# Performance work log

Measured on AMD Instinct MI355X. Metric: run time of the kernel, lower is better.

## Reference

```python
import jax, jax.numpy as jnp
import numpy as np

N_NODES = 100000
N_REL = 8
IN_DIM = 64
HID = 128
OUT = 64
N_EDGES = 640000


def setup_inputs() -> dict:
    key = jax.random.key(0)
    ks = jax.random.split(key, 24)

    def w(k, shape, fan_in):
        return jax.random.normal(k, shape, jnp.float32) / np.sqrt(fan_in).astype(np.float32)

    inp = {}
    inp["emb"] = jax.random.normal(ks[0], (N_NODES, IN_DIM), jnp.float32)
    dims = [(IN_DIM, HID), (HID, HID), (HID, HID // 2), (HID // 2, OUT)]
    for i, (di, do) in enumerate(dims, 1):
        inp[f"W{i}"] = w(ks[3 * i], (N_REL, di, do), di)      # per-relation weight
        inp[f"R{i}"] = w(ks[3 * i + 1], (di, do), di)          # root weight
        inp[f"B{i}"] = jnp.zeros((do,), jnp.float32)           # bias
    inp["g1"] = jnp.ones((HID,), jnp.float32)
    inp["b1"] = jnp.zeros((HID,), jnp.float32)
    inp["g2"] = jnp.ones((HID,), jnp.float32)
    inp["b2"] = jnp.zeros((HID,), jnp.float32)
    inp["ei"] = jax.random.randint(ks[20], (2, N_EDGES), 0, N_NODES, jnp.int32)
    inp["et"] = jax.random.randint(ks[21], (N_EDGES,), 0, N_REL, jnp.int32)
    return inp


def rgcn(x, ei, et, W, Wr, b):
    # PyG RGCNConv (aggr='mean'): out_i = x_i @ Wroot + b + sum_r mean_{j in N_r(i)} x_j @ W_r
    # Aggregate-then-transform: mean x[src] per (dst, rel) bin, then per-relation GEMM.
    n, r, d = x.shape[0], W.shape[0], x.shape[1]
    src, dst = ei[0], ei[1]
    seg = dst * r + et                                   # combined (node, relation) segment id
    agg = jax.ops.segment_sum(x[src], seg, num_segments=n * r)          # [N*R, d]
    cnt = jax.ops.segment_sum(jnp.ones((src.shape[0],), x.dtype), seg, num_segments=n * r)
    agg = (agg / jnp.maximum(cnt, 1.0)[:, None]).reshape(n, r, d)       # mean per relation
    return jnp.einsum('nri,rio->no', agg, W) + x @ Wr + b


def layer_norm(x, g, b, eps=1e-5):
    mu = jnp.mean(x, axis=-1, keepdims=True)
    var = jnp.mean((x - mu) ** 2, axis=-1, keepdims=True)
    return (x - mu) * jax.lax.rsqrt(var + eps) * g + b


def reference(emb, W1, R1, B1, W2, R2, B2, W3, R3, B3, W4, R4, B4, g1, b1, g2, b2, ei, et):
    # dropout is eval-mode identity
    x = jax.nn.relu(rgcn(emb, ei, et, W1, R1, B1))
    x = layer_norm(x, g1, b1)
    identity = x
    x = jax.nn.relu(rgcn(x, ei, et, W2, R2, B2))
    x = layer_norm(x + identity, g2, b2)
    x = jax.nn.relu(rgcn(x, ei, et, W3, R3, B3))
    return rgcn(x, ei, et, W4, R4, B4)
```

## Files before the change

kernel.cpp:

```cpp
#include <hip/hip_runtime.h>
#include <math.h>

#define NN 100000
#define NR 8
#define NE 640000
#define SEGN (NN * NR)
#define SPB 2048
#define NSB ((SEGN + SPB - 1) / SPB)

#define QSZ 25024
static const int qbase[5] = {0, 25024, 50048, 75072, 100032};
static const int qsize[4] = {25024, 25024, 25024, 24960};

typedef __attribute__((ext_vector_type(8))) __bf16 bf16x8;
typedef __attribute__((ext_vector_type(4))) float  f32x4;

__device__ __forceinline__ float bf2f(unsigned short b) {
    return __uint_as_float((unsigned)b << 16);
}
__device__ __forceinline__ unsigned short f2bf(float v) {
    __bf16 b = (__bf16)v;
    return __builtin_bit_cast(unsigned short, b);
}


__global__ __launch_bounds__(256) void count_kernel(
    const int* __restrict__ dst, const int* __restrict__ et, unsigned* __restrict__ cnt) {
    int e = blockIdx.x * 256 + threadIdx.x;
    if (e < NE) atomicAdd(&cnt[(size_t)et[e] * NN + dst[e]], 1u);
}

__global__ __launch_bounds__(256) void scan1_kernel(
    const unsigned* __restrict__ cnt, unsigned* __restrict__ bsum) {
    __shared__ unsigned red[256];
    int b = blockIdx.x, t = threadIdx.x;
    int i0 = b * SPB;
    unsigned s = 0;
#pragma unroll
    for (int k = 0; k < SPB / 256; ++k) {
        int i = i0 + k * 256 + t;
        if (i < SEGN) s += cnt[i];
    }
    red[t] = s;
    __syncthreads();
    for (int off = 128; off >= 1; off >>= 1) {
        if (t < off) red[t] += red[t + off];
        __syncthreads();
    }
    if (t == 0) bsum[b] = red[0];
}

__global__ __launch_bounds__(512) void scan2_kernel(
    unsigned* __restrict__ bsum, int* __restrict__ segoff) {
    __shared__ unsigned buf[512];
    int t = threadIdx.x;
    unsigned v = (t < NSB) ? bsum[t] : 0u;
    buf[t] = v;
    __syncthreads();
    for (int off = 1; off < 512; off <<= 1) {
        unsigned w = (t >= off) ? buf[t - off] : 0u;
        __syncthreads();
        buf[t] += w;
        __syncthreads();
    }
    if (t < NSB) bsum[t] = buf[t] - v;
    if (t == 0) segoff[SEGN] = NE;
}

__global__ __launch_bounds__(256) void scan3_kernel(
    const unsigned* __restrict__ cnt, const unsigned* __restrict__ bsum,
    int* __restrict__ segoff) {
    __shared__ unsigned lc[SPB];
    __shared__ unsigned tsum[256];
    int b = blockIdx.x, t = threadIdx.x;
    int i0 = b * SPB;
#pragma unroll
    for (int k = 0; k < SPB / 256; ++k) {
        int i = i0 + k * 256 + t;
        lc[k * 256 + t] = (i < SEGN) ? cnt[i] : 0u;
    }
    __syncthreads();
    unsigned s = 0;
#pragma unroll
    for (int k = 0; k < 8; ++k) s += lc[t * 8 + k];
    tsum[t] = s;
    __syncthreads();
    for (int off = 1; off < 256; off <<= 1) {
        unsigned w = (t >= off) ? tsum[t - off] : 0u;
        __syncthreads();
        tsum[t] += w;
        __syncthreads();
    }
    unsigned base = bsum[b] + tsum[t] - s;
#pragma unroll
    for (int k = 0; k < 8; ++k) {
        unsigned c = lc[t * 8 + k];
        lc[t * 8 + k] = base;
        base += c;
    }
    __syncthreads();
#pragma unroll
    for (int k = 0; k < SPB / 256; ++k) {
        int i = i0 + k * 256 + t;
        if (i < SEGN) segoff[i] = (int)lc[k * 256 + t];
    }
}

__global__ __launch_bounds__(256) void fill_kernel(
    const int* __restrict__ src, const int* __restrict__ dst, const int* __restrict__ et,
    const int* __restrict__ segoff, unsigned* __restrict__ cursor, int* __restrict__ esrc) {
    int e = blockIdx.x * 256 + threadIdx.x;
    if (e >= NE) return;
    int d = dst[e];
    int seg = et[e] * NN + d;
    int pos = segoff[seg] + (int)atomicAdd(&cursor[seg], 1u);
    esrc[pos] = src[e] | ((d & 3) << 17);
}

__global__ __launch_bounds__(256) void conv_emb(
    const float* __restrict__ emb, ushort* __restrict__ embb) {
    int i = blockIdx.x * 256 + threadIdx.x;
    if (i * 4 >= NN * 64) return;
    f32x4 v = *(const f32x4*)(emb + (size_t)i * 4);
    ushort4 o;
    o.x = f2bf(v[0]); o.y = f2bf(v[1]); o.z = f2bf(v[2]); o.w = f2bf(v[3]);
    *(ushort4*)(embb + (size_t)i * 4) = o;
}


template <int D, int O>
__global__ __launch_bounds__(256) void pack_kernel(
    const float* __restrict__ W, const float* __restrict__ Wr, __bf16* __restrict__ Wp) {
    constexpr int KT = D / 32, NTN = O / 16;
    int idx = blockIdx.x * 256 + threadIdx.x;
    if (idx >= (NR + 1) * KT * NTN * 64) return;
    int l = idx & 63;
    int rest = idx >> 6;
    int nt = rest % NTN; rest /= NTN;
    int kt = rest % KT;
    int r  = rest / KT;
    const float* srcw = (r < NR) ? (W + (size_t)r * D * O) : Wr;
    int n  = nt * 16 + (l & 15);
    int k0 = kt * 32 + (l >> 4) * 8;
    bf16x8 v;
#pragma unroll
    for (int j = 0; j < 8; ++j) {
        int p  = k0 + j;
        int kd = (D == 128) ? ((p >> 1) + ((p & 1) << 6)) : p;
        v[j] = (__bf16)srcw[(size_t)kd * O + n];
    }
    *(bf16x8*)(Wp + (size_t)idx * 8) = v;
}


template <int D, int O, int MODE, int XF, int OF>
__global__ __launch_bounds__(256) void fused_kernel(
    int mb,
    const ushort* __restrict__ aggG, const __bf16* __restrict__ Wp,
    const float* __restrict__ bias, const float* __restrict__ gamma,
    const float* __restrict__ beta, const unsigned* __restrict__ xres,
    const void* __restrict__ xroot, void* __restrict__ outv, int gbase, int gQP,
    const void* __restrict__ xin, const int* __restrict__ segoff,
    const int* __restrict__ esrc, ushort* __restrict__ aggS, int nbase, int sQP)
{
    constexpr int KT = D / 32, NTN = O / 16;
    int tid = threadIdx.x;
    int wv = tid >> 6, ln = tid & 63;

    if ((int)blockIdx.x < mb) {
        constexpr int PD = (D == 64) ? 8 : 3;
        int lg = ln >> 4, lm = ln & 15;
        int i0 = blockIdx.x * 64 + wv * 16;

        const ushort* abase = aggG + ((size_t)(i0 + lm)) * D + lg * 8;

        bf16x8 Aall[NR][KT];
#pragma unroll
        for (int r = 0; r < PD; ++r) {
            const ushort* ar = abase + (size_t)r * gQP * D;
#pragma unroll
            for (int kt = 0; kt < KT; ++kt)
                Aall[r][kt] = *(const bf16x8*)(ar + kt * 32);
        }

        bf16x8 Aroot[KT];
        {
            int nrow = gbase + i0 + lm;
            if (nrow >= NN) nrow = NN - 1;
#pragma unroll
            for (int kt = 0; kt < KT; ++kt) {
                if constexpr (XF == 1) {
                    Aroot[kt] = *(const bf16x8*)((const ushort*)xroot +
                                                 (size_t)nrow * 128 + kt * 32 + lg * 8);
                } else {
                    Aroot[kt] = *(const bf16x8*)((const ushort*)xroot +
                                                 (size_t)nrow * 64 + kt * 32 + lg * 8);
                }
            }
        }

        f32x4 acc[NTN];
#pragma unroll
        for (int nt = 0; nt < NTN; ++nt)
#pragma unroll
            for (int q = 0; q < 4; ++q) acc[nt][q] = 0.0f;

#pragma unroll
        for (int r = 0; r < NR; ++r) {
            if (r + PD < NR) {
                const ushort* an = abase + (size_t)(r + PD) * gQP * D;
#pragma unroll
                for (int kt = 0; kt < KT; ++kt)
                    Aall[r + PD][kt] = *(const bf16x8*)(an + kt * 32);
            }
            const __bf16* bp = Wp + (((size_t)(r * KT) * NTN) << 9) + (ln << 3);
#pragma unroll
            for (int kt = 0; kt < KT; ++kt) {
                const __bf16* bpk = bp + (((size_t)(kt * NTN)) << 9);
#pragma unroll
                for (int nt = 0; nt < NTN; ++nt) {
                    bf16x8 B = *(const bf16x8*)(bpk + ((size_t)nt << 9));
                    acc[nt] = __builtin_amdgcn_mfma_f32_16x16x32_bf16(Aall[r][kt], B, acc[nt], 0, 0, 0);
                }
            }
        }
        {
            const __bf16* bp = Wp + (((size_t)(8 * KT) * NTN) << 9) + (ln << 3);
#pragma unroll
            for (int kt = 0; kt < KT; ++kt) {
                const __bf16* bpk = bp + (((size_t)(kt * NTN)) << 9);
#pragma unroll
                for (int nt = 0; nt < NTN; ++nt) {
                    bf16x8 B = *(const bf16x8*)(bpk + ((size_t)nt << 9));
                    acc[nt] = __builtin_amdgcn_mfma_f32_16x16x32_bf16(Aroot[kt], B, acc[nt], 0, 0, 0);
                }
            }
        }

        float bb[NTN], gg[NTN], be[NTN];
#pragma unroll
        for (int nt = 0; nt < NTN; ++nt) {
            bb[nt] = bias[nt * 16 + lm];
            if constexpr (MODE <= 1) {
                gg[nt] = gamma[nt * 16 + lm];
                be[nt] = beta[nt * 16 + lm];
            } else {
                gg[nt] = 0.0f; be[nt] = 0.0f;
            }
        }
#pragma unroll
        for (int q = 0; q < 4; ++q) {
            int row = lg * 4 + q;
            int n = gbase + i0 + row;
            int nc = (n < NN) ? n : 0;
            float v[NTN];
#pragma unroll
            for (int nt = 0; nt < NTN; ++nt) {
                v[nt] = acc[nt][q] + bb[nt];
                if constexpr (MODE <= 2) v[nt] = fmaxf(v[nt], 0.0f);
                if constexpr (MODE == 1) {
                    unsigned w = xres[(size_t)nc * 64 + (nt & 3) * 16 + lm];
                    v[nt] += bf2f((unsigned short)((nt < 4) ? (w & 0xFFFFu) : (w >> 16)));
                }
            }
            if constexpr (MODE <= 1) {
                float s1 = 0.0f, s2 = 0.0f;
#pragma unroll
                for (int nt = 0; nt < NTN; ++nt) { s1 += v[nt]; s2 += v[nt] * v[nt]; }
#pragma unroll
                for (int off = 1; off < 16; off <<= 1) {
                    s1 += __shfl_xor(s1, off, 64);
                    s2 += __shfl_xor(s2, off, 64);
                }
                float mu  = s1 * (1.0f / O);
                float var = s2 * (1.0f / O) - mu * mu;
                float rs  = rsqrtf(var + 1e-5f);
#pragma unroll
                for (int nt = 0; nt < NTN; ++nt) v[nt] = (v[nt] - mu) * rs * gg[nt] + be[nt];
            }
            if (n < NN) {
                if constexpr (OF == 0) {
#pragma unroll
                    for (int nt = 0; nt < NTN; ++nt)
                        __builtin_nontemporal_store(
                            v[nt], (float*)outv + (size_t)n * O + nt * 16 + lm);
                } else if constexpr (OF == 1) {
#pragma unroll
                    for (int nt = 0; nt < 4; ++nt)
                        ((unsigned*)outv)[(size_t)n * 64 + nt * 16 + lm] =
                            (unsigned)f2bf(v[nt]) | ((unsigned)f2bf(v[nt + 4]) << 16);
                } else {
#pragma unroll
                    for (int nt = 0; nt < NTN; ++nt)
                        ((ushort*)outv)[(size_t)n * 64 + nt * 16 + lm] = f2bf(v[nt]);
                }
            }
        }
        return;
    }

    int gb = blockIdx.x - mb;
    int tile = gb >> 3, r = gb & 7;
    int i0 = tile * 16 + wv * 4;
    int n0 = nbase + i0;

    const ushort*   xb = (const ushort*)xin;
    const unsigned* xs = (const unsigned*)xin;

    float ax[4] = {0, 0, 0, 0}, ay[4] = {0, 0, 0, 0};
    int eo[5];
#pragma unroll
    for (int k = 0; k <= 4; ++k) {
        int node = n0 + k; if (node > NN) node = NN;
        eo[k] = segoff[r * NN + node];
    }
    for (int ei = eo[0]; ei < eo[4]; ei += 4) {
        int nb = eo[4] - ei; if (nb > 4) nb = 4;
        int mm[4]; float vx[4], vy[4];
#pragma unroll
        for (int b = 0; b < 4; ++b) mm[b] = (b < nb) ? esrc[ei + b] : 0;
#pragma unroll
        for (int b = 0; b < 4; ++b) {
            if (b < nb) {
                int s = mm[b] & 0x1FFFF;
                if constexpr (XF == 1) {
                    unsigned w = xs[(size_t)s * 64 + ln];
                    vx[b] = bf2f((unsigned short)(w & 0xFFFFu));
                    vy[b] = bf2f((unsigned short)(w >> 16));
                } else {
                    vx[b] = bf2f(xb[(size_t)s * 64 + ln]);
                }
            }
        }
#pragma unroll
        for (int b = 0; b < 4; ++b) {
            if (b < nb) {
                int k = mm[b] >> 17;
#pragma unroll
                for (int kk = 0; kk < 4; ++kk) {
                    ax[kk] += (kk == k) ? vx[b] : 0.0f;
                    if constexpr (D == 128) ay[kk] += (kk == k) ? vy[b] : 0.0f;
                }
            }
        }
    }
#pragma unroll
    for (int k = 0; k < 4; ++k) {
        int c = eo[k + 1] - eo[k];
        float sc = (c > 0) ? 1.0f / (float)c : 0.0f;
        size_t row = ((size_t)r * sQP + i0 + k) * D;
        if constexpr (D == 128) {
            unsigned st = (unsigned)f2bf(ax[k] * sc) | ((unsigned)f2bf(ay[k] * sc) << 16);
            *((unsigned*)(aggS + row) + ln) = st;
        } else {
            aggS[row + ln] = f2bf(ax[k] * sc);
        }
    }
}


#define SLOTE(D) ((size_t)8 * 25024 * (D))

template <int D, int O, int MODE, int XF, int OF>
static void run_layer(const void* xin, const __bf16* Wp, const float* bias,
                      const float* gamma, const float* beta, const unsigned* xres,
                      void* out, ushort* agg, const int* segoff, const int* esrc,
                      hipStream_t stream) {
    auto slot = [&](int q) { return agg + (size_t)(q & 1) * SLOTE(D); };
    auto gB = [](int n) { return (n / 16) * 8; };
    auto mB = [](int n) { return n / 64; };
    fused_kernel<D, O, MODE, XF, OF><<<gB(qsize[0]), 256, 0, stream>>>(
        0, nullptr, Wp, bias, gamma, beta, xres, xin, out, 0, 0,
        xin, segoff, esrc, slot(0), qbase[0], qsize[0]);
    for (int q = 0; q < 3; ++q) {
        fused_kernel<D, O, MODE, XF, OF><<<mB(qsize[q]) + gB(qsize[q + 1]), 256, 0, stream>>>(
            mB(qsize[q]), slot(q), Wp, bias, gamma, beta, xres, xin, out,
            qbase[q], qsize[q],
            xin, segoff, esrc, slot(q + 1), qbase[q + 1], qsize[q + 1]);
    }
    fused_kernel<D, O, MODE, XF, OF><<<mB(qsize[3]), 256, 0, stream>>>(
        mB(qsize[3]), slot(3), Wp, bias, gamma, beta, xres, xin, out,
        qbase[3], qsize[3],
        xin, segoff, esrc, slot(3), 0, 0);
}

extern "C" void kernel_launch(void* const* d_in, const int* in_sizes, int n_in,
                              void* d_out, int out_size, void* d_ws, size_t ws_size,
                              hipStream_t stream) {
    const float* emb = (const float*)d_in[0];
    const float* W1  = (const float*)d_in[1];
    const float* R1  = (const float*)d_in[2];
    const float* B1  = (const float*)d_in[3];
    const float* W2  = (const float*)d_in[4];
    const float* R2  = (const float*)d_in[5];
    const float* B2  = (const float*)d_in[6];
    const float* W3  = (const float*)d_in[7];
    const float* R3  = (const float*)d_in[8];
    const float* B3  = (const float*)d_in[9];
    const float* W4  = (const float*)d_in[10];
    const float* R4  = (const float*)d_in[11];
    const float* B4  = (const float*)d_in[12];
    const float* g1  = (const float*)d_in[13];
    const float* b1  = (const float*)d_in[14];
    const float* g2  = (const float*)d_in[15];
    const float* b2  = (const float*)d_in[16];
    const int*   ei  = (const int*)d_in[17];
    const int*   et  = (const int*)d_in[18];
    const int* srcp = ei;
    const int* dstp = ei + NE;

    char* ws = (char*)d_ws;
    if (ws_size < 185721872u) return;
    int*      segoff = (int*)(ws + 0);
    int*      esrc   = (int*)(ws + 3200016);
    __bf16*   Wp1    = (__bf16*)(ws + 5760016);
    __bf16*   Wp2    = (__bf16*)(ws + 5907472);
    __bf16*   Wp3    = (__bf16*)(ws + 6202384);
    __bf16*   Wp4    = (__bf16*)(ws + 6349840);
    ushort*   embb   = (ushort*)(ws + 6423568);
    void*     x1     = (void*)(ws + 19223568);
    void*     x2     = (void*)(ws + 44823568);
    void*     x3     = (void*)(ws + 70423568);
    ushort*   agg    = (ushort*)(ws + 83223568);
    unsigned* cnt    = (unsigned*)(ws + 83223568);
    unsigned* cursor = (unsigned*)(ws + 86423568);
    unsigned* bsum   = (unsigned*)(ws + 89623568);
    float*    outp   = (float*)d_out;

    hipMemsetAsync(cnt, 0, 3200000, stream);
    hipMemsetAsync(cursor, 0, 3200000, stream);

    count_kernel<<<(NE + 255) / 256, 256, 0, stream>>>(dstp, et, cnt);
    scan1_kernel<<<NSB, 256, 0, stream>>>(cnt, bsum);
    scan2_kernel<<<1, 512, 0, stream>>>(bsum, segoff);
    scan3_kernel<<<NSB, 256, 0, stream>>>(cnt, bsum, segoff);
    fill_kernel<<<(NE + 255) / 256, 256, 0, stream>>>(
        srcp, dstp, et, segoff, cursor, esrc);
    conv_emb<<<(NN * 64 / 4 + 255) / 256, 256, 0, stream>>>(emb, embb);

    pack_kernel<64, 128><<<(9 * 2 * 8 * 64 + 255) / 256, 256, 0, stream>>>(W1, R1, Wp1);
    pack_kernel<128, 128><<<(9 * 4 * 8 * 64 + 255) / 256, 256, 0, stream>>>(W2, R2, Wp2);
    pack_kernel<128, 64><<<(9 * 4 * 4 * 64 + 255) / 256, 256, 0, stream>>>(W3, R3, Wp3);
    pack_kernel<64, 64><<<(9 * 2 * 4 * 64 + 255) / 256, 256, 0, stream>>>(W4, R4, Wp4);

    run_layer<64, 128, 0, 2, 1>(embb, Wp1, B1, g1, b1, nullptr, x1,
                                agg, segoff, esrc, stream);
    run_layer<128, 128, 1, 1, 1>(x1, Wp2, B2, g2, b2, (const unsigned*)x1, x2,
                                 agg, segoff, esrc, stream);
    run_layer<128, 64, 2, 1, 2>(x2, Wp3, B3, nullptr, nullptr, nullptr, x3,
                                agg, segoff, esrc, stream);
    run_layer<64, 64, 3, 2, 0>(x3, Wp4, B4, nullptr, nullptr, nullptr, outp,
                               agg, segoff, esrc, stream);
}
```

Before: 853.5 us.

## Split fused gather+GEMM pipeline into separate gather and GEMM kernels per quarter

```diff
diff --git a/kernel.cpp b/kernel.cpp
--- a/kernel.cpp
+++ b/kernel.cpp
@@ -8,7 +8,6 @@
 #define SPB 2048
 #define NSB ((SEGN + SPB - 1) / SPB)
 
-#define QSZ 25024
 static const int qbase[5] = {0, 25024, 50048, 75072, 100032};
 static const int qsize[4] = {25024, 25024, 25024, 24960};
 
@@ -111,10 +110,9 @@
     const int* __restrict__ segoff, unsigned* __restrict__ cursor, int* __restrict__ esrc) {
     int e = blockIdx.x * 256 + threadIdx.x;
     if (e >= NE) return;
-    int d = dst[e];
-    int seg = et[e] * NN + d;
+    int seg = et[e] * NN + dst[e];
     int pos = segoff[seg] + (int)atomicAdd(&cursor[seg], 1u);
-    esrc[pos] = src[e] | ((d & 3) << 17);
+    esrc[pos] = src[e];
 }
 
 __global__ __launch_bounds__(256) void conv_emb(
@@ -153,155 +151,15 @@
 }
 
 
-template <int D, int O, int MODE, int XF, int OF>
-__global__ __launch_bounds__(256) void fused_kernel(
-    int mb,
-    const ushort* __restrict__ aggG, const __bf16* __restrict__ Wp,
-    const float* __restrict__ bias, const float* __restrict__ gamma,
-    const float* __restrict__ beta, const unsigned* __restrict__ xres,
-    const void* __restrict__ xroot, void* __restrict__ outv, int gbase, int gQP,
+template <int D, int XF>
+__global__ __launch_bounds__(256) void gather_kernel(
     const void* __restrict__ xin, const int* __restrict__ segoff,
-    const int* __restrict__ esrc, ushort* __restrict__ aggS, int nbase, int sQP)
+    const int* __restrict__ esrc, ushort* __restrict__ agg,
+    int nbase, int QP)
 {
-    constexpr int KT = D / 32, NTN = O / 16;
-    int tid = threadIdx.x;
-    int wv = tid >> 6, ln = tid & 63;
-
-    if ((int)blockIdx.x < mb) {
-        constexpr int PD = (D == 64) ? 8 : 3;
-        int lg = ln >> 4, lm = ln & 15;
-        int i0 = blockIdx.x * 64 + wv * 16;
-
-        const ushort* abase = aggG + ((size_t)(i0 + lm)) * D + lg * 8;
-
-        bf16x8 Aall[NR][KT];
-#pragma unroll
-        for (int r = 0; r < PD; ++r) {
-            const ushort* ar = abase + (size_t)r * gQP * D;
-#pragma unroll
-            for (int kt = 0; kt < KT; ++kt)
-                Aall[r][kt] = *(const bf16x8*)(ar + kt * 32);
-        }
-
-        bf16x8 Aroot[KT];
-        {
-            int nrow = gbase + i0 + lm;
-            if (nrow >= NN) nrow = NN - 1;
-#pragma unroll
-            for (int kt = 0; kt < KT; ++kt) {
-                if constexpr (XF == 1) {
-                    Aroot[kt] = *(const bf16x8*)((const ushort*)xroot +
-                                                 (size_t)nrow * 128 + kt * 32 + lg * 8);
-                } else {
-                    Aroot[kt] = *(const bf16x8*)((const ushort*)xroot +
-                                                 (size_t)nrow * 64 + kt * 32 + lg * 8);
-                }
-            }
-        }
-
-        f32x4 acc[NTN];
-#pragma unroll
-        for (int nt = 0; nt < NTN; ++nt)
-#pragma unroll
-            for (int q = 0; q < 4; ++q) acc[nt][q] = 0.0f;
-
-#pragma unroll
-        for (int r = 0; r < NR; ++r) {
-            if (r + PD < NR) {
-                const ushort* an = abase + (size_t)(r + PD) * gQP * D;
-#pragma unroll
-                for (int kt = 0; kt < KT; ++kt)
-                    Aall[r + PD][kt] = *(const bf16x8*)(an + kt * 32);
-            }
-            const __bf16* bp = Wp + (((size_t)(r * KT) * NTN) << 9) + (ln << 3);
-#pragma unroll
-            for (int kt = 0; kt < KT; ++kt) {
-                const __bf16* bpk = bp + (((size_t)(kt * NTN)) << 9);
-#pragma unroll
-                for (int nt = 0; nt < NTN; ++nt) {
-                    bf16x8 B = *(const bf16x8*)(bpk + ((size_t)nt << 9));
-                    acc[nt] = __builtin_amdgcn_mfma_f32_16x16x32_bf16(Aall[r][kt], B, acc[nt], 0, 0, 0);
-                }
-            }
-        }
-        {
-            const __bf16* bp = Wp + (((size_t)(8 * KT) * NTN) << 9) + (ln << 3);
-#pragma unroll
-            for (int kt = 0; kt < KT; ++kt) {
-                const __bf16* bpk = bp + (((size_t)(kt * NTN)) << 9);
-#pragma unroll
-                for (int nt = 0; nt < NTN; ++nt) {
-                    bf16x8 B = *(const bf16x8*)(bpk + ((size_t)nt << 9));
-                    acc[nt] = __builtin_amdgcn_mfma_f32_16x16x32_bf16(Aroot[kt], B, acc[nt], 0, 0, 0);
-                }
-            }
-        }
-
-        float bb[NTN], gg[NTN], be[NTN];
-#pragma unroll
-        for (int nt = 0; nt < NTN; ++nt) {
-            bb[nt] = bias[nt * 16 + lm];
-            if constexpr (MODE <= 1) {
-                gg[nt] = gamma[nt * 16 + lm];
-                be[nt] = beta[nt * 16 + lm];
-            } else {
-                gg[nt] = 0.0f; be[nt] = 0.0f;
-            }
-        }
-#pragma unroll
-        for (int q = 0; q < 4; ++q) {
-            int row = lg * 4 + q;
-            int n = gbase + i0 + row;
-            int nc = (n < NN) ? n : 0;
-            float v[NTN];
-#pragma unroll
-            for (int nt = 0; nt < NTN; ++nt) {
-                v[nt] = acc[nt][q] + bb[nt];
-                if constexpr (MODE <= 2) v[nt] = fmaxf(v[nt], 0.0f);
-                if constexpr (MODE == 1) {
-                    unsigned w = xres[(size_t)nc * 64 + (nt & 3) * 16 + lm];
-                    v[nt] += bf2f((unsigned short)((nt < 4) ? (w & 0xFFFFu) : (w >> 16)));
-                }
-            }
-            if constexpr (MODE <= 1) {
-                float s1 = 0.0f, s2 = 0.0f;
-#pragma unroll
-                for (int nt = 0; nt < NTN; ++nt) { s1 += v[nt]; s2 += v[nt] * v[nt]; }
-#pragma unroll
-                for (int off = 1; off < 16; off <<= 1) {
-                    s1 += __shfl_xor(s1, off, 64);
-                    s2 += __shfl_xor(s2, off, 64);
-                }
-                float mu  = s1 * (1.0f / O);
-                float var = s2 * (1.0f / O) - mu * mu;
-                float rs  = rsqrtf(var + 1e-5f);
-#pragma unroll
-                for (int nt = 0; nt < NTN; ++nt) v[nt] = (v[nt] - mu) * rs * gg[nt] + be[nt];
-            }
-            if (n < NN) {
-                if constexpr (OF == 0) {
-#pragma unroll
-                    for (int nt = 0; nt < NTN; ++nt)
-                        __builtin_nontemporal_store(
-                            v[nt], (float*)outv + (size_t)n * O + nt * 16 + lm);
-                } else if constexpr (OF == 1) {
-#pragma unroll
-                    for (int nt = 0; nt < 4; ++nt)
-                        ((unsigned*)outv)[(size_t)n * 64 + nt * 16 + lm] =
-                            (unsigned)f2bf(v[nt]) | ((unsigned)f2bf(v[nt + 4]) << 16);
-                } else {
-#pragma unroll
-                    for (int nt = 0; nt < NTN; ++nt)
-                        ((ushort*)outv)[(size_t)n * 64 + nt * 16 + lm] = f2bf(v[nt]);
-                }
-            }
-        }
-        return;
-    }
-
-    int gb = blockIdx.x - mb;
-    int tile = gb >> 3, r = gb & 7;
-    int i0 = tile * 16 + wv * 4;
+    int wv = threadIdx.x >> 6, ln = threadIdx.x & 63;
+    int r  = blockIdx.y;
+    int i0 = blockIdx.x * 16 + wv * 4;
     int n0 = nbase + i0;
 
     const ushort*   xb = (const ushort*)xin;
@@ -314,33 +172,32 @@
         int node = n0 + k; if (node > NN) node = NN;
         eo[k] = segoff[r * NN + node];
     }
-    for (int ei = eo[0]; ei < eo[4]; ei += 4) {
-        int nb = eo[4] - ei; if (nb > 4) nb = 4;
-        int mm[4]; float vx[4], vy[4];
-#pragma unroll
-        for (int b = 0; b < 4; ++b) mm[b] = (b < nb) ? esrc[ei + b] : 0;
+    for (int e4 = eo[0]; e4 < eo[4]; e4 += 4) {
+        int nb = eo[4] - e4; if (nb > 4) nb = 4;
+        int ss[4]; float vx[4], vy[4];
+#pragma unroll
+        for (int b = 0; b < 4; ++b) ss[b] = (b < nb) ? esrc[e4 + b] : 0;
 #pragma unroll
         for (int b = 0; b < 4; ++b) {
             if (b < nb) {
-                int s = mm[b] & 0x1FFFF;
                 if constexpr (XF == 1) {
-                    unsigned w = xs[(size_t)s * 64 + ln];
+                    unsigned w = xs[(size_t)ss[b] * 64 + ln];
                     vx[b] = bf2f((unsigned short)(w & 0xFFFFu));
                     vy[b] = bf2f((unsigned short)(w >> 16));
                 } else {
-                    vx[b] = bf2f(xb[(size_t)s * 64 + ln]);
+                    vx[b] = bf2f(xb[(size_t)ss[b] * 64 + ln]);
                 }
             }
         }
 #pragma unroll
         for (int b = 0; b < 4; ++b) {
             if (b < nb) {
-                int k = mm[b] >> 17;
-#pragma unroll
-                for (int kk = 0; kk < 4; ++kk) {
-                    ax[kk] += (kk == k) ? vx[b] : 0.0f;
-                    if constexpr (D == 128) ay[kk] += (kk == k) ? vy[b] : 0.0f;
-                }
+                int e = e4 + b;
+                int k = (e >= eo[1]) + (e >= eo[2]) + (e >= eo[3]);
+                if (k == 0)      { ax[0] += vx[b]; if constexpr (D == 128) ay[0] += vy[b]; }
+                else if (k == 1) { ax[1] += vx[b]; if constexpr (D == 128) ay[1] += vy[b]; }
+                else if (k == 2) { ax[2] += vx[b]; if constexpr (D == 128) ay[2] += vy[b]; }
+                else             { ax[3] += vx[b]; if constexpr (D == 128) ay[3] += vy[b]; }
             }
         }
     }
@@ -348,40 +205,167 @@
     for (int k = 0; k < 4; ++k) {
         int c = eo[k + 1] - eo[k];
         float sc = (c > 0) ? 1.0f / (float)c : 0.0f;
-        size_t row = ((size_t)r * sQP + i0 + k) * D;
+        size_t row = ((size_t)r * QP + i0 + k) * D;
         if constexpr (D == 128) {
             unsigned st = (unsigned)f2bf(ax[k] * sc) | ((unsigned)f2bf(ay[k] * sc) << 16);
-            *((unsigned*)(aggS + row) + ln) = st;
+            *((unsigned*)(agg + row) + ln) = st;
         } else {
-            aggS[row + ln] = f2bf(ax[k] * sc);
-        }
-    }
-}
-
-
-#define SLOTE(D) ((size_t)8 * 25024 * (D))
+            agg[row + ln] = f2bf(ax[k] * sc);
+        }
+    }
+}
+
+
+template <int D, int O, int MODE, int XF, int OF>
+__global__ __launch_bounds__(64) void gemm_layer(
+    const ushort* __restrict__ agg, const __bf16* __restrict__ Wp,
+    const float* __restrict__ bias, const float* __restrict__ gamma,
+    const float* __restrict__ beta, const unsigned* __restrict__ xres,
+    const void* __restrict__ xroot, void* __restrict__ outv, int base, int QP)
+{
+    constexpr int KT = D / 32, NTN = O / 16;
+    constexpr int PD = (D == 64) ? 8 : 3;
+    int ln = threadIdx.x, lg = ln >> 4, lm = ln & 15;
+    int i0 = blockIdx.x * 16;
+
+    const ushort* abase = agg + ((size_t)(i0 + lm)) * D + lg * 8;
+
+    bf16x8 Aall[NR][KT];
+#pragma unroll
+    for (int r = 0; r < PD; ++r) {
+        const ushort* ar = abase + (size_t)r * QP * D;
+#pragma unroll
+        for (int kt = 0; kt < KT; ++kt)
+            Aall[r][kt] = *(const bf16x8*)(ar + kt * 32);
+    }
+
+    bf16x8 Aroot[KT];
+    {
+        int nrow = base + i0 + lm;
+        if (nrow >= NN) nrow = NN - 1;
+#pragma unroll
+        for (int kt = 0; kt < KT; ++kt) {
+            if constexpr (XF == 1) {
+                Aroot[kt] = *(const bf16x8*)((const ushort*)xroot +
+                                             (size_t)nrow * 128 + kt * 32 + lg * 8);
+            } else {
+                Aroot[kt] = *(const bf16x8*)((const ushort*)xroot +
+                                             (size_t)nrow * 64 + kt * 32 + lg * 8);
+            }
+        }
+    }
+
+    f32x4 acc[NTN];
+#pragma unroll
+    for (int nt = 0; nt < NTN; ++nt)
+#pragma unroll
+        for (int q = 0; q < 4; ++q) acc[nt][q] = 0.0f;
+
+#pragma unroll
+    for (int r = 0; r < NR; ++r) {
+        if (r + PD < NR) {
+            const ushort* an = abase + (size_t)(r + PD) * QP * D;
+#pragma unroll
+            for (int kt = 0; kt < KT; ++kt)
+                Aall[r + PD][kt] = *(const bf16x8*)(an + kt * 32);
+        }
+        const __bf16* bp = Wp + (((size_t)(r * KT) * NTN) << 9) + (ln << 3);
+#pragma unroll
+        for (int kt = 0; kt < KT; ++kt) {
+            const __bf16* bpk = bp + (((size_t)(kt * NTN)) << 9);
+#pragma unroll
+            for (int nt = 0; nt < NTN; ++nt) {
+                bf16x8 B = *(const bf16x8*)(bpk + ((size_t)nt << 9));
+                acc[nt] = __builtin_amdgcn_mfma_f32_16x16x32_bf16(Aall[r][kt], B, acc[nt], 0, 0, 0);
+            }
+        }
+    }
+    {
+        const __bf16* bp = Wp + (((size_t)(8 * KT) * NTN) << 9) + (ln << 3);
+#pragma unroll
+        for (int kt = 0; kt < KT; ++kt) {
+            const __bf16* bpk = bp + (((size_t)(kt * NTN)) << 9);
+#pragma unroll
+            for (int nt = 0; nt < NTN; ++nt) {
+                bf16x8 B = *(const bf16x8*)(bpk + ((size_t)nt << 9));
+                acc[nt] = __builtin_amdgcn_mfma_f32_16x16x32_bf16(Aroot[kt], B, acc[nt], 0, 0, 0);
+            }
+        }
+    }
+
+    float bb[NTN], gg[NTN], be[NTN];
+#pragma unroll
+    for (int nt = 0; nt < NTN; ++nt) {
+        bb[nt] = bias[nt * 16 + lm];
+        if constexpr (MODE <= 1) {
+            gg[nt] = gamma[nt * 16 + lm];
+            be[nt] = beta[nt * 16 + lm];
+        } else {
+            gg[nt] = 0.0f; be[nt] = 0.0f;
+        }
+    }
+#pragma unroll
+    for (int q = 0; q < 4; ++q) {
+        int row = lg * 4 + q;
+        int n = base + i0 + row;
+        int nc = (n < NN) ? n : 0;
+        float v[NTN];
+#pragma unroll
+        for (int nt = 0; nt < NTN; ++nt) {
+            v[nt] = acc[nt][q] + bb[nt];
+            if constexpr (MODE <= 2) v[nt] = fmaxf(v[nt], 0.0f);
+            if constexpr (MODE == 1) {
+                unsigned w = xres[(size_t)nc * 64 + (nt & 3) * 16 + lm];
+                v[nt] += bf2f((unsigned short)((nt < 4) ? (w & 0xFFFFu) : (w >> 16)));
+            }
+        }
+        if constexpr (MODE <= 1) {
+            float s1 = 0.0f, s2 = 0.0f;
+#pragma unroll
+            for (int nt = 0; nt < NTN; ++nt) { s1 += v[nt]; s2 += v[nt] * v[nt]; }
+#pragma unroll
+            for (int off = 1; off < 16; off <<= 1) {
+                s1 += __shfl_xor(s1, off, 64);
+                s2 += __shfl_xor(s2, off, 64);
+            }
+            float mu  = s1 * (1.0f / O);
+            float var = s2 * (1.0f / O) - mu * mu;
+            float rs  = rsqrtf(var + 1e-5f);
+#pragma unroll
+            for (int nt = 0; nt < NTN; ++nt) v[nt] = (v[nt] - mu) * rs * gg[nt] + be[nt];
+        }
+        if (n < NN) {
+            if constexpr (OF == 0) {
+#pragma unroll
+                for (int nt = 0; nt < NTN; ++nt)
+                    __builtin_nontemporal_store(
+                        v[nt], (float*)outv + (size_t)n * O + nt * 16 + lm);
+            } else if constexpr (OF == 1) {
+#pragma unroll
+                for (int nt = 0; nt < 4; ++nt)
+                    ((unsigned*)outv)[(size_t)n * 64 + nt * 16 + lm] =
+                        (unsigned)f2bf(v[nt]) | ((unsigned)f2bf(v[nt + 4]) << 16);
+            } else {
+#pragma unroll
+                for (int nt = 0; nt < NTN; ++nt)
+                    ((ushort*)outv)[(size_t)n * 64 + nt * 16 + lm] = f2bf(v[nt]);
+            }
+        }
+    }
+}
+
 
 template <int D, int O, int MODE, int XF, int OF>
 static void run_layer(const void* xin, const __bf16* Wp, const float* bias,
                       const float* gamma, const float* beta, const unsigned* xres,
                       void* out, ushort* agg, const int* segoff, const int* esrc,
                       hipStream_t stream) {
-    auto slot = [&](int q) { return agg + (size_t)(q & 1) * SLOTE(D); };
-    auto gB = [](int n) { return (n / 16) * 8; };
-    auto mB = [](int n) { return n / 64; };
-    fused_kernel<D, O, MODE, XF, OF><<<gB(qsize[0]), 256, 0, stream>>>(
-        0, nullptr, Wp, bias, gamma, beta, xres, xin, out, 0, 0,
-        xin, segoff, esrc, slot(0), qbase[0], qsize[0]);
-    for (int q = 0; q < 3; ++q) {
-        fused_kernel<D, O, MODE, XF, OF><<<mB(qsize[q]) + gB(qsize[q + 1]), 256, 0, stream>>>(
-            mB(qsize[q]), slot(q), Wp, bias, gamma, beta, xres, xin, out,
-            qbase[q], qsize[q],
-            xin, segoff, esrc, slot(q + 1), qbase[q + 1], qsize[q + 1]);
-    }
-    fused_kernel<D, O, MODE, XF, OF><<<mB(qsize[3]), 256, 0, stream>>>(
-        mB(qsize[3]), slot(3), Wp, bias, gamma, beta, xres, xin, out,
-        qbase[3], qsize[3],
-        xin, segoff, esrc, slot(3), 0, 0);
+    for (int q = 0; q < 4; ++q) {
+        gather_kernel<D, XF><<<dim3(qsize[q] / 16, 8), 256, 0, stream>>>(
+            xin, segoff, esrc, agg, qbase[q], qsize[q]);
+        gemm_layer<D, O, MODE, XF, OF><<<qsize[q] / 16, 64, 0, stream>>>(
+            agg, Wp, bias, gamma, beta, xres, xin, out, qbase[q], qsize[q]);
+    }
 }
 
 extern "C" void kernel_launch(void* const* d_in, const int* in_sizes, int n_in,
@@ -410,7 +394,7 @@
     const int* dstp = ei + NE;
 
     char* ws = (char*)d_ws;
-    if (ws_size < 185721872u) return;
+    if (ws_size < 134472720u) return;
     int*      segoff = (int*)(ws + 0);
     int*      esrc   = (int*)(ws + 3200016);
     __bf16*   Wp1    = (__bf16*)(ws + 5760016);
```

After: 867.9 us. No clear change (+1.7%).
